# Kernel tuning notes

Hardware: AMD Instinct MI355X
Metric: run time of the kernel (lower is better)

The kernel has to match this reference:

```python
import jax, jax.numpy as jnp
import numpy as np

NUM_HEADS = 16  # matches init_kwargs


def _linear(x, W, b):
    # torch nn.Linear: x @ W.T + b
    return jnp.matmul(x, W.T) + b


def setup_inputs() -> dict:
    key = jax.random.key(0)
    ks = jax.random.split(key, 5)
    B, S, Dm = 8, 2048, 1024
    scale = 0.02
    return {
        "q": jax.random.normal(ks[0], (B, S, Dm), dtype=jnp.float32),
        "k": jax.random.normal(ks[1], (B, S, Dm), dtype=jnp.float32),
        "v": jax.random.normal(ks[2], (B, S, Dm), dtype=jnp.float32),
        "W": jax.random.normal(ks[3], (Dm, Dm), dtype=jnp.float32) * scale,
        "b": jax.random.normal(ks[4], (Dm,), dtype=jnp.float32) * scale,
    }


def reference(q, k, v, W, b):
    B, S, Dm = q.shape
    H = NUM_HEADS
    D = Dm // H  # head_dim

    def proj(x):
        # linear -> view(B, S, H, D) -> transpose(2, 3): (B, S, D, H)
        # NOTE: original code transposes dims 2 and 3 (head_dim <-> heads),
        # NOT the usual (1, 2); we reproduce that exactly.
        y = _linear(x, W, b).reshape(B, S, H, D)
        return jnp.swapaxes(y, 2, 3)  # (B, S, D, H)

    qh, kh, vh = proj(q), proj(k), proj(v)

    # scores: (B, S, D, H) @ (B, S, H, D) -> (B, S, D, D), scaled by sqrt(head_dim)
    logits = jnp.einsum("bsdh,bseh->bsde", qh, kh) / jnp.sqrt(jnp.float32(D))
    attn = jax.nn.softmax(logits, axis=-1)
    out = jnp.einsum("bsde,bseh->bsdh", attn, vh)  # (B, S, D, H)

    # transpose(1, 2) -> (B, D, S, H), then view(B, -1, model_dim)
    concat = jnp.swapaxes(out, 1, 2).reshape(B, -1, Dm)  # (B, S, Dm)
    return _linear(concat, W, b)
```

## Files before the change

### kernel.cpp

```cpp
#include <hip/hip_runtime.h>
#include <hip/hip_fp16.h>
#include <math.h>

typedef _Float16 f16;
typedef _Float16 half8_t __attribute__((ext_vector_type(8)));
typedef _Float16 half4_t __attribute__((ext_vector_type(4)));
typedef _Float16 half2_t __attribute__((ext_vector_type(2)));
typedef __fp16   fp16x2  __attribute__((ext_vector_type(2)));
typedef float    float4_t __attribute__((ext_vector_type(4)));

__device__ f16 Wh[1024 * 1024];
__device__ f16 Xh[3ul * 16777216];

__device__ __forceinline__ void gl_lds16(const void* g, void* l) {
    __builtin_amdgcn_global_load_lds(
        (const __attribute__((address_space(1))) void*)g,
        (__attribute__((address_space(3))) void*)l,
        16, 0, 0);
}

__device__ __forceinline__ half2_t pkrtz(float a, float b) {
    fp16x2 r = __builtin_amdgcn_cvt_pkrtz(a, b);
    return __builtin_bit_cast(half2_t, r);
}

__device__ __forceinline__ half8_t cvt8(float4_t lo, float4_t hi) {
    half2_t p0 = pkrtz(lo[0], lo[1]);
    half2_t p1 = pkrtz(lo[2], lo[3]);
    half2_t p2 = pkrtz(hi[0], hi[1]);
    half2_t p3 = pkrtz(hi[2], hi[3]);
    half8_t r;
    r[0] = p0[0]; r[1] = p0[1]; r[2] = p1[0]; r[3] = p1[1];
    r[4] = p2[0]; r[5] = p2[1]; r[6] = p3[0]; r[7] = p3[1];
    return r;
}

__global__ __launch_bounds__(256) void convert_w_kernel(const float* __restrict__ W) {
    const int i = (blockIdx.x * 256 + threadIdx.x) * 8;
    const float4_t a = *(const float4_t*)(W + i);
    const float4_t b = *(const float4_t*)(W + i + 4);
    half8_t h;
#pragma unroll
    for (int t = 0; t < 4; ++t) h[t] = (f16)a[t];
#pragma unroll
    for (int t = 0; t < 4; ++t) h[4 + t] = (f16)b[t];
    *(half8_t*)(Wh + i) = h;
}

__global__ __launch_bounds__(256) void convert_x_kernel(
    const float* __restrict__ q, const float* __restrict__ k,
    const float* __restrict__ v)
{
    const int z = blockIdx.z;
    const float* src = (z == 0) ? q : (z == 1) ? k : v;
    f16* dst = Xh + (size_t)z * 16777216;
    const size_t i = ((size_t)blockIdx.x * 256 + threadIdx.x) * 8;
    const float4_t a = *(const float4_t*)(src + i);
    const float4_t b = *(const float4_t*)(src + i + 4);
    *(half8_t*)(dst + i) = cvt8(a, b);
}


__device__ __forceinline__ void stage_half(const f16* __restrict__ base, f16* dst,
                                           int tid, int kt, int half) {
#pragma unroll
    for (int it = 2 * half; it < 2 * half + 2; ++it) {
        const int ch = tid + it * 512;
        const int r = ch >> 3, s = ch & 7;
        gl_lds16(base + (size_t)r * 1024 + kt + ((s ^ (r & 7)) << 3), dst + ch * 8);
    }
}

template <typename TC>
__device__ __forceinline__ void gemm_tile256(const f16* __restrict__ A,
                                             const float* __restrict__ bias,
                                             TC* __restrict__ C,
                                             int row0, int col0) {
    constexpr int K = 1024, N = 1024, NT = 16;
    __shared__ __align__(16) f16 smem[65536];
    f16* const Asb = smem;
    f16* const Bsb = smem + 32768;

    const int tid  = threadIdx.x;
    const int lane = tid & 63;
    const int wave = tid >> 6;
    const int wr   = wave >> 2;
    const int wc   = wave & 3;
    const int lrow = lane & 15;
    const int kq   = lane >> 4;

    const f16* const Ag = A + (size_t)row0 * K;
    const f16* const Bg = Wh + (size_t)col0 * K;

    float4_t acc[8][4];
#pragma unroll
    for (int i = 0; i < 8; ++i)
#pragma unroll
        for (int j = 0; j < 4; ++j)
            acc[i][j] = (float4_t){0.f, 0.f, 0.f, 0.f};

    stage_half(Ag, Asb, tid, 0, 0);
    stage_half(Ag, Asb, tid, 0, 1);
    stage_half(Bg, Bsb, tid, 0, 0);
    stage_half(Bg, Bsb, tid, 0, 1);
    stage_half(Ag, Asb + 16384, tid, 64, 0);
    stage_half(Ag, Asb + 16384, tid, 64, 1);

    for (int u = 0; u < NT; ++u) {
        const int c = u & 1;
        const f16* const Ac = Asb + (c << 14);
        const f16* const Bc = Bsb + (c << 14);
        f16* const Bn = Bsb + ((c ^ 1) << 14);
        f16* const Af = Asb + (c << 14);
        const int k1 = ((u + 1) & (NT - 1)) * 64;
        const int k2 = ((u + 2) & (NT - 1)) * 64;

        half8_t afv[8][2], bfv[4][2];

        stage_half(Bg, Bn, tid, k1, 0);
        asm volatile("s_waitcnt vmcnt(6)" ::: "memory");
        __builtin_amdgcn_s_barrier();
#pragma unroll
        for (int i = 0; i < 4; ++i) {
            const int m = wr * 128 + i * 16 + lrow;
#pragma unroll
            for (int ks = 0; ks < 2; ++ks)
                afv[i][ks] = *(const half8_t*)(Ac + m * 64 + (((ks * 4 + kq) ^ (m & 7)) << 3));
        }
#pragma unroll
        for (int j = 0; j < 2; ++j) {
            const int n = wc * 64 + j * 16 + lrow;
#pragma unroll
            for (int ks = 0; ks < 2; ++ks)
                bfv[j][ks] = *(const half8_t*)(Bc + n * 64 + (((ks * 4 + kq) ^ (n & 7)) << 3));
        }
        __builtin_amdgcn_s_setprio(1);
#pragma unroll
        for (int i = 0; i < 4; ++i)
#pragma unroll
            for (int j = 0; j < 2; ++j)
#pragma unroll
                for (int ks = 0; ks < 2; ++ks)
                    acc[i][j] = __builtin_amdgcn_mfma_f32_16x16x32_f16(
                        afv[i][ks], bfv[j][ks], acc[i][j], 0, 0, 0);
        __builtin_amdgcn_s_setprio(0);
        __builtin_amdgcn_s_barrier();

#pragma unroll
        for (int i = 4; i < 8; ++i) {
            const int m = wr * 128 + i * 16 + lrow;
#pragma unroll
            for (int ks = 0; ks < 2; ++ks)
                afv[i][ks] = *(const half8_t*)(Ac + m * 64 + (((ks * 4 + kq) ^ (m & 7)) << 3));
        }
#pragma unroll
        for (int j = 2; j < 4; ++j) {
            const int n = wc * 64 + j * 16 + lrow;
#pragma unroll
            for (int ks = 0; ks < 2; ++ks)
                bfv[j][ks] = *(const half8_t*)(Bc + n * 64 + (((ks * 4 + kq) ^ (n & 7)) << 3));
        }
        stage_half(Bg, Bn, tid, k1, 1);
        __builtin_amdgcn_s_barrier();
        __builtin_amdgcn_s_setprio(1);
#pragma unroll
        for (int i = 0; i < 4; ++i)
#pragma unroll
            for (int j = 2; j < 4; ++j)
#pragma unroll
                for (int ks = 0; ks < 2; ++ks)
                    acc[i][j] = __builtin_amdgcn_mfma_f32_16x16x32_f16(
                        afv[i][ks], bfv[j][ks], acc[i][j], 0, 0, 0);
        __builtin_amdgcn_s_setprio(0);
        asm volatile("s_waitcnt lgkmcnt(0)" ::: "memory");
        __builtin_amdgcn_s_barrier();

        stage_half(Ag, Af, tid, k2, 0);
        __builtin_amdgcn_s_barrier();
        __builtin_amdgcn_s_setprio(1);
#pragma unroll
        for (int i = 4; i < 8; ++i)
#pragma unroll
            for (int j = 0; j < 2; ++j)
#pragma unroll
                for (int ks = 0; ks < 2; ++ks)
                    acc[i][j] = __builtin_amdgcn_mfma_f32_16x16x32_f16(
                        afv[i][ks], bfv[j][ks], acc[i][j], 0, 0, 0);
        __builtin_amdgcn_s_setprio(0);
        __builtin_amdgcn_s_barrier();

        stage_half(Ag, Af, tid, k2, 1);
        __builtin_amdgcn_s_barrier();
        __builtin_amdgcn_s_setprio(1);
#pragma unroll
        for (int i = 4; i < 8; ++i)
#pragma unroll
            for (int j = 2; j < 4; ++j)
#pragma unroll
                for (int ks = 0; ks < 2; ++ks)
                    acc[i][j] = __builtin_amdgcn_mfma_f32_16x16x32_f16(
                        afv[i][ks], bfv[j][ks], acc[i][j], 0, 0, 0);
        __builtin_amdgcn_s_setprio(0);
        __builtin_amdgcn_s_barrier();
    }
    asm volatile("s_waitcnt vmcnt(0)" ::: "memory");
    __builtin_amdgcn_s_barrier();

    const int ccol  = lane & 15;
    const int rbase = (lane >> 4) << 2;

    if constexpr (sizeof(TC) == 2) {
        f16* const Cs = smem;
#pragma unroll
        for (int j = 0; j < 4; ++j) {
            const int gcol = wc * 64 + j * 16 + ccol;
            const float bv = bias[col0 + gcol];
#pragma unroll
            for (int i = 0; i < 8; ++i) {
                const int grow = wr * 128 + i * 16 + rbase;
                const int cx = gcol ^ (((grow >> 2) & 3) << 4);
#pragma unroll
                for (int r = 0; r < 4; ++r)
                    Cs[(grow + r) * 256 + cx] = (f16)(acc[i][j][r] + bv);
            }
        }
        __builtin_amdgcn_s_barrier();
#pragma unroll
        for (int p = 0; p < 16; ++p) {
            const int idx = tid + p * 512;
            const int row = idx >> 5;
            const int col = (idx & 31) * 8;
            const int cx  = col ^ (((row >> 2) & 3) << 4);
            const half8_t v = *(const half8_t*)(Cs + row * 256 + cx);
            *(half8_t*)((TC*)C + (size_t)(row0 + row) * N + col0 + col) = v;
        }
    } else {
#pragma unroll
        for (int j = 0; j < 4; ++j) {
            const int gcol = col0 + wc * 64 + j * 16 + ccol;
            const float bv = bias[gcol];
#pragma unroll
            for (int i = 0; i < 8; ++i) {
#pragma unroll
                for (int r = 0; r < 4; ++r) {
                    const int grow = row0 + wr * 128 + i * 16 + rbase + r;
                    C[(size_t)grow * N + gcol] = (TC)(acc[i][j][r] + bv);
                }
            }
        }
    }
}

template <typename TC>
__global__ __launch_bounds__(512, 2) void gemm_kernel(
    const f16* __restrict__ A, const float* __restrict__ bias,
    TC* __restrict__ C) {
    const int f    = blockIdx.x + 64 * blockIdx.y;
    const int virt = (f & 7) * 32 + (f >> 3);
    gemm_tile256<TC>(A, bias, C, ((virt >> 2) & 63) * 256, (virt & 3) * 256);
}

__global__ __launch_bounds__(512, 2) void gemm_proj_kernel(
    const float* __restrict__ bias,
    f16* __restrict__ cq, f16* __restrict__ ck, f16* __restrict__ cv) {
    const int f    = blockIdx.x + 64 * (blockIdx.y + 4 * blockIdx.z);
    const int virt = (f & 7) * 96 + (f >> 3);
    const int y = virt & 3, x = (virt >> 2) & 63, z = virt >> 8;
    f16* C = (z == 0) ? cq : (z == 1) ? ck : cv;
    gemm_tile256<f16>(Xh + (size_t)z * 16777216, bias, C, x * 256, y * 256);
}

__global__ __launch_bounds__(256) void attn_kernel(
    const f16* __restrict__ pq, const f16* __restrict__ pk,
    const f16* __restrict__ pv, f16* __restrict__ outp)
{
    __shared__ __align__(16) f16 Qs[4][64][24];
    __shared__ __align__(16) f16 Ks[4][64][24];
    __shared__ __align__(16) f16 Vs[4][16][72];
    __shared__ __align__(16) f16 Os[4][64][24];
    const int lane = threadIdx.x & 63;
    const int wave = threadIdx.x >> 6;
    const int p0 = blockIdx.x * 4;
    const int p = p0 + wave;
    const f16* qptr = pq + (size_t)p * 1024;
    const f16* kptr = pk + (size_t)p * 1024;
    const f16* vptr = pv + (size_t)p * 1024;

    {
        const int h  = lane >> 2;
        const int c0 = (lane & 3) << 4;
        const half8_t q0 = *(const half8_t*)(qptr + lane * 16);
        const half8_t q1 = *(const half8_t*)(qptr + lane * 16 + 8);
        const half8_t k0 = *(const half8_t*)(kptr + lane * 16);
        const half8_t k1 = *(const half8_t*)(kptr + lane * 16 + 8);
#pragma unroll
        for (int t = 0; t < 8; ++t) {
            Qs[wave][c0 + t][h]     = q0[t];
            Qs[wave][c0 + 8 + t][h] = q1[t];
            Ks[wave][c0 + t][h]     = k0[t];
            Ks[wave][c0 + 8 + t][h] = k1[t];
        }
        const half8_t v0 = *(const half8_t*)(vptr + lane * 16);
        const half8_t v1 = *(const half8_t*)(vptr + lane * 16 + 8);
        *(half8_t*)&Vs[wave][h][c0]     = v0;
        *(half8_t*)&Vs[wave][h][c0 + 8] = v1;
    }
    __syncthreads();

    const int g  = lane >> 4;
    const int lc = lane & 15;

    half4_t ka[4], qb[4];
#pragma unroll
    for (int t = 0; t < 4; ++t) {
        ka[t] = *(const half4_t*)&Ks[wave][16 * t + lc][4 * g];
        qb[t] = *(const half4_t*)&Qs[wave][16 * t + lc][4 * g];
    }
    float4_t s[4][4];
#pragma unroll
    for (int et = 0; et < 4; ++et)
#pragma unroll
        for (int dt = 0; dt < 4; ++dt)
            s[et][dt] = __builtin_amdgcn_mfma_f32_16x16x16f16(
                ka[et], qb[dt], (float4_t){0.f, 0.f, 0.f, 0.f}, 0, 0, 0);

    float inv[4];
#pragma unroll
    for (int dt = 0; dt < 4; ++dt) {
        float m = s[0][dt][0];
#pragma unroll
        for (int et = 0; et < 4; ++et)
#pragma unroll
            for (int r = 0; r < 4; ++r) m = fmaxf(m, s[et][dt][r]);
        m = fmaxf(m, __shfl_xor(m, 16));
        m = fmaxf(m, __shfl_xor(m, 32));
        float sum = 0.f;
#pragma unroll
        for (int et = 0; et < 4; ++et)
#pragma unroll
            for (int r = 0; r < 4; ++r) {
                const float t = __expf((s[et][dt][r] - m) * 0.125f);
                s[et][dt][r] = t;
                sum += t;
            }
        sum += __shfl_xor(sum, 16);
        sum += __shfl_xor(sum, 32);
        inv[dt] = 1.f / sum;
    }

    half4_t pa[4][4];
#pragma unroll
    for (int kt = 0; kt < 4; ++kt)
#pragma unroll
        for (int dt = 0; dt < 4; ++dt) {
            const half2_t lo = pkrtz(s[kt][dt][0] * inv[dt], s[kt][dt][1] * inv[dt]);
            const half2_t hi = pkrtz(s[kt][dt][2] * inv[dt], s[kt][dt][3] * inv[dt]);
            half4_t f;
            f[0] = lo[0]; f[1] = lo[1]; f[2] = hi[0]; f[3] = hi[1];
            pa[kt][dt] = f;
        }

    float4_t o[4];
#pragma unroll
    for (int dt = 0; dt < 4; ++dt) o[dt] = (float4_t){0.f, 0.f, 0.f, 0.f};
#pragma unroll
    for (int kt = 0; kt < 4; ++kt) {
        const half4_t vb = *(const half4_t*)&Vs[wave][lc][16 * kt + 4 * g];
#pragma unroll
        for (int dt = 0; dt < 4; ++dt)
            o[dt] = __builtin_amdgcn_mfma_f32_16x16x16f16(pa[kt][dt], vb, o[dt], 0, 0, 0);
    }

#pragma unroll
    for (int dt = 0; dt < 4; ++dt)
#pragma unroll
        for (int r = 0; r < 4; ++r)
            Os[wave][16 * dt + 4 * g + r][lc] = (f16)o[dt][r];
    __syncthreads();

    const int b0 = p0 >> 11;
    const int s0 = p0 & 2047;
#pragma unroll
    for (int hf = 0; hf < 2; ++hf) {
        const int u  = threadIdx.x + hf * 256;
        const int d  = u >> 3;
        const int si = (u >> 1) & 3;
        const int uh = u & 1;
        const half8_t val = *(const half8_t*)&Os[si][d][uh * 8];
        f16* dst = outp + ((size_t)(b0 * 64 + d) * 2048 + (s0 + si)) * 16 + uh * 8;
        *(half8_t*)dst = val;
    }
}

extern "C" void kernel_launch(void* const* d_in, const int* in_sizes, int n_in,
                              void* d_out, int out_size, void* d_ws, size_t ws_size,
                              hipStream_t stream)
{
    const float* q    = (const float*)d_in[0];
    const float* k    = (const float*)d_in[1];
    const float* v    = (const float*)d_in[2];
    const float* W    = (const float*)d_in[3];
    const float* bias = (const float*)d_in[4];
    float* out = (float*)d_out;

    const int M = 16384;
    const size_t elems = (size_t)M * 1024;

    f16* projq = (f16*)d_ws;
    f16* attn  = projq + elems;
    f16* projk = (f16*)d_out;
    f16* projv = projk + elems;

    convert_w_kernel<<<512, 256, 0, stream>>>(W);
    dim3 gridc(8192, 1, 3);
    convert_x_kernel<<<gridc, 256, 0, stream>>>(q, k, v);

    dim3 gridp(M / 256, 1024 / 256, 3);
    gemm_proj_kernel<<<gridp, 512, 0, stream>>>(bias, projq, projk, projv);
    attn_kernel<<<M / 4, 256, 0, stream>>>(projq, projk, projv, attn);
    dim3 gridf(M / 256, 1024 / 256);
    gemm_kernel<float><<<gridf, 512, 0, stream>>>(attn, bias, out);
}
```

Before: 415.6 us.

## Reorder GEMM main loop into quadrant-wise LDS reads interleaved with async stages

Restructures the GEMM inner loop so each of the four MFMA quadrants is preceded by loading only the fragments it newly needs (A rows 0-3, A rows 4-7, B cols 2-3), reusing already-loaded fragments across quadrants. Global-to-LDS stage calls are spread one per quadrant, and the vmcnt wait moves to the end of each iteration with an extra prologue wait. Explicit lgkmcnt waits and sched_barriers pin the ordering. The aim is better overlap of LDS reads, global loads and MFMA work, at the risk of stricter scheduling and changed wait/barrier correctness.

```diff
diff --git a/kernel.cpp b/kernel.cpp
--- a/kernel.cpp
+++ b/kernel.cpp
@@ -105,6 +105,8 @@
     stage_half(Bg, Bsb, tid, 0, 1);
     stage_half(Ag, Asb + 16384, tid, 64, 0);
     stage_half(Ag, Asb + 16384, tid, 64, 1);
+    asm volatile("s_waitcnt vmcnt(4)" ::: "memory");
+    __builtin_amdgcn_s_barrier();
 
     for (int u = 0; u < NT; ++u) {
         const int c = u & 1;
@@ -115,25 +117,26 @@
         const int k1 = ((u + 1) & (NT - 1)) * 64;
         const int k2 = ((u + 2) & (NT - 1)) * 64;
 
-        half8_t afv[8][2], bfv[4][2];
-
-        stage_half(Bg, Bn, tid, k1, 0);
-        asm volatile("s_waitcnt vmcnt(6)" ::: "memory");
-        __builtin_amdgcn_s_barrier();
+        half8_t am0[4][2], am1[4][2], bn0[2][2], bn1[2][2];
+
 #pragma unroll
         for (int i = 0; i < 4; ++i) {
             const int m = wr * 128 + i * 16 + lrow;
 #pragma unroll
             for (int ks = 0; ks < 2; ++ks)
-                afv[i][ks] = *(const half8_t*)(Ac + m * 64 + (((ks * 4 + kq) ^ (m & 7)) << 3));
+                am0[i][ks] = *(const half8_t*)(Ac + m * 64 + (((ks * 4 + kq) ^ (m & 7)) << 3));
         }
 #pragma unroll
         for (int j = 0; j < 2; ++j) {
             const int n = wc * 64 + j * 16 + lrow;
 #pragma unroll
             for (int ks = 0; ks < 2; ++ks)
-                bfv[j][ks] = *(const half8_t*)(Bc + n * 64 + (((ks * 4 + kq) ^ (n & 7)) << 3));
-        }
+                bn0[j][ks] = *(const half8_t*)(Bc + n * 64 + (((ks * 4 + kq) ^ (n & 7)) << 3));
+        }
+        stage_half(Bg, Bn, tid, k1, 0);
+        __builtin_amdgcn_s_barrier();
+        asm volatile("s_waitcnt lgkmcnt(0)" ::: "memory");
+        __builtin_amdgcn_sched_barrier(0);
         __builtin_amdgcn_s_setprio(1);
 #pragma unroll
         for (int i = 0; i < 4; ++i)
@@ -142,65 +145,69 @@
 #pragma unroll
                 for (int ks = 0; ks < 2; ++ks)
                     acc[i][j] = __builtin_amdgcn_mfma_f32_16x16x32_f16(
-                        afv[i][ks], bfv[j][ks], acc[i][j], 0, 0, 0);
+                        am0[i][ks], bn0[j][ks], acc[i][j], 0, 0, 0);
         __builtin_amdgcn_s_setprio(0);
         __builtin_amdgcn_s_barrier();
 
 #pragma unroll
-        for (int i = 4; i < 8; ++i) {
-            const int m = wr * 128 + i * 16 + lrow;
+        for (int i = 0; i < 4; ++i) {
+            const int m = wr * 128 + (4 + i) * 16 + lrow;
 #pragma unroll
             for (int ks = 0; ks < 2; ++ks)
-                afv[i][ks] = *(const half8_t*)(Ac + m * 64 + (((ks * 4 + kq) ^ (m & 7)) << 3));
-        }
-#pragma unroll
-        for (int j = 2; j < 4; ++j) {
-            const int n = wc * 64 + j * 16 + lrow;
+                am1[i][ks] = *(const half8_t*)(Ac + m * 64 + (((ks * 4 + kq) ^ (m & 7)) << 3));
+        }
+        stage_half(Bg, Bn, tid, k1, 1);
+        __builtin_amdgcn_s_barrier();
+        asm volatile("s_waitcnt lgkmcnt(0)" ::: "memory");
+        __builtin_amdgcn_sched_barrier(0);
+        __builtin_amdgcn_s_setprio(1);
+#pragma unroll
+        for (int i = 0; i < 4; ++i)
+#pragma unroll
+            for (int j = 0; j < 2; ++j)
+#pragma unroll
+                for (int ks = 0; ks < 2; ++ks)
+                    acc[4 + i][j] = __builtin_amdgcn_mfma_f32_16x16x32_f16(
+                        am1[i][ks], bn0[j][ks], acc[4 + i][j], 0, 0, 0);
+        __builtin_amdgcn_s_setprio(0);
+        __builtin_amdgcn_s_barrier();
+
+#pragma unroll
+        for (int j = 0; j < 2; ++j) {
+            const int n = wc * 64 + (2 + j) * 16 + lrow;
 #pragma unroll
             for (int ks = 0; ks < 2; ++ks)
-                bfv[j][ks] = *(const half8_t*)(Bc + n * 64 + (((ks * 4 + kq) ^ (n & 7)) << 3));
-        }
-        stage_half(Bg, Bn, tid, k1, 1);
-        __builtin_amdgcn_s_barrier();
+                bn1[j][ks] = *(const half8_t*)(Bc + n * 64 + (((ks * 4 + kq) ^ (n & 7)) << 3));
+        }
+        stage_half(Ag, Af, tid, k2, 0);
+        __builtin_amdgcn_s_barrier();
+        asm volatile("s_waitcnt lgkmcnt(0)" ::: "memory");
+        __builtin_amdgcn_sched_barrier(0);
         __builtin_amdgcn_s_setprio(1);
 #pragma unroll
         for (int i = 0; i < 4; ++i)
 #pragma unroll
-            for (int j = 2; j < 4; ++j)
+            for (int j = 0; j < 2; ++j)
 #pragma unroll
                 for (int ks = 0; ks < 2; ++ks)
-                    acc[i][j] = __builtin_amdgcn_mfma_f32_16x16x32_f16(
-                        afv[i][ks], bfv[j][ks], acc[i][j], 0, 0, 0);
+                    acc[i][2 + j] = __builtin_amdgcn_mfma_f32_16x16x32_f16(
+                        am0[i][ks], bn1[j][ks], acc[i][2 + j], 0, 0, 0);
         __builtin_amdgcn_s_setprio(0);
-        asm volatile("s_waitcnt lgkmcnt(0)" ::: "memory");
-        __builtin_amdgcn_s_barrier();
-
-        stage_half(Ag, Af, tid, k2, 0);
+        __builtin_amdgcn_s_barrier();
+
+        stage_half(Ag, Af, tid, k2, 1);
         __builtin_amdgcn_s_barrier();
         __builtin_amdgcn_s_setprio(1);
 #pragma unroll
-        for (int i = 4; i < 8; ++i)
+        for (int i = 0; i < 4; ++i)
 #pragma unroll
             for (int j = 0; j < 2; ++j)
 #pragma unroll
                 for (int ks = 0; ks < 2; ++ks)
-                    acc[i][j] = __builtin_amdgcn_mfma_f32_16x16x32_f16(
-                        afv[i][ks], bfv[j][ks], acc[i][j], 0, 0, 0);
+                    acc[4 + i][2 + j] = __builtin_amdgcn_mfma_f32_16x16x32_f16(
+                        am1[i][ks], bn1[j][ks], acc[4 + i][2 + j], 0, 0, 0);
         __builtin_amdgcn_s_setprio(0);
-        __builtin_amdgcn_s_barrier();
-
-        stage_half(Ag, Af, tid, k2, 1);
-        __builtin_amdgcn_s_barrier();
-        __builtin_amdgcn_s_setprio(1);
-#pragma unroll
-        for (int i = 4; i < 8; ++i)
-#pragma unroll
-            for (int j = 2; j < 4; ++j)
-#pragma unroll
-                for (int ks = 0; ks < 2; ++ks)
-                    acc[i][j] = __builtin_amdgcn_mfma_f32_16x16x32_f16(
-                        afv[i][ks], bfv[j][ks], acc[i][j], 0, 0, 0);
-        __builtin_amdgcn_s_setprio(0);
+        asm volatile("s_waitcnt vmcnt(4)" ::: "memory");
         __builtin_amdgcn_s_barrier();
     }
     asm volatile("s_waitcnt vmcnt(0)" ::: "memory");
```

Measured after the change: 413.3 us. About the same (-0.5%).
